# Performance work log

Hardware: AMD Instinct MI355X
Metric: run time of the kernel (lower is better)

The kernel has to match this reference:

```python
import jax, jax.numpy as jnp
import numpy as np

B, S, D = 4, 2048, 512
H = 8
DEPTH = D // H  # 64


def setup_inputs() -> dict:
    key = jax.random.key(0)
    ks = jax.random.split(key, 6)
    scale = 1.0 / np.sqrt(D)
    return {
        "x": jax.random.normal(ks[0], (B, S, D), dtype=jnp.float32),
        "y": jax.random.normal(ks[1], (B, S, D), dtype=jnp.float32),
        "W_q": jax.random.normal(ks[2], (D, D), dtype=jnp.float32) * scale,
        "W_k": jax.random.normal(ks[3], (D, D), dtype=jnp.float32) * scale,
        "W_v": jax.random.normal(ks[4], (D, D), dtype=jnp.float32) * scale,
        "W_o": jax.random.normal(ks[5], (D, D), dtype=jnp.float32) * scale,
    }


def _split_heads(t):
    # [B, S, D] -> [B, H, S, DEPTH]
    b, s, _ = t.shape
    return t.reshape(b, s, H, DEPTH).transpose(0, 2, 1, 3)


def reference(x, y, W_q, W_k, W_v, W_o):
    q = _split_heads(x @ W_q) * (DEPTH ** -0.5)   # [B,H,Sq,d]
    k = _split_heads(y @ W_k)                      # [B,H,Sk,d]
    v = _split_heads(y @ W_v)                      # [B,H,Sk,d]
    logits = jnp.einsum("bhqd,bhkd->bhqk", q, k)   # [B,H,Sq,Sk]
    weights = jax.nn.softmax(logits, axis=-1)
    attn = jnp.einsum("bhqk,bhkd->bhqd", weights, v)  # [B,H,Sq,d]
    attn = attn.transpose(0, 2, 1, 3).reshape(x.shape[0], x.shape[1], D)
    return attn @ W_o
```

## Files before the change

### kernel.cpp

```cpp
#include <hip/hip_runtime.h>
#include <hip/hip_bf16.h>
#include <math.h>
#include <stdint.h>

#define NB 4
#define NS 2048
#define ND 512
#define NH 8
#define DEP 64

typedef __attribute__((ext_vector_type(8))) short bf16x8;
typedef __attribute__((ext_vector_type(4))) short bf16x4;
typedef __attribute__((ext_vector_type(4))) float f32x4;

#define QSCALE 0.18033688011112042f

__device__ __forceinline__ short f2b(float f) {
  unsigned u = __float_as_uint(f);
  u += 0x7FFF + ((u >> 16) & 1);
  return (short)(u >> 16);
}
__device__ __forceinline__ unsigned pk2(float a, float b) {
  union { __hip_bfloat162 h; unsigned u; } c;
  c.h = __float22bfloat162_rn(float2{a, b});
  return c.u;
}

__global__ __launch_bounds__(256) void cast_xy(const float* __restrict__ x,
                                               const float* __restrict__ y,
                                               short* __restrict__ xb,
                                               short* __restrict__ yb) {
  const float* src = blockIdx.y ? y : x;
  short* dst = blockIdx.y ? yb : xb;
  size_t i = ((size_t)blockIdx.x * 256 + threadIdx.x) * 4;
  float4 v = *(const float4*)(src + i);
  bf16x4 o;
  o[0] = f2b(v.x); o[1] = f2b(v.y); o[2] = f2b(v.z); o[3] = f2b(v.w);
  *(bf16x4*)(dst + i) = o;
}

__global__ __launch_bounds__(256) void trans_w(
    const float* __restrict__ W0, const float* __restrict__ W1,
    const float* __restrict__ W2, const float* __restrict__ W3,
    short* __restrict__ T0, short* __restrict__ T1, short* __restrict__ T2,
    short* __restrict__ T3) {
  const float* W = blockIdx.z == 0 ? W0 : blockIdx.z == 1 ? W1
                   : blockIdx.z == 2 ? W2 : W3;
  short* T = blockIdx.z == 0 ? T0 : blockIdx.z == 1 ? T1
             : blockIdx.z == 2 ? T2 : T3;
  __shared__ float tile[64][65];
  const int t = threadIdx.x;
  const int k0 = blockIdx.x * 64, n0 = blockIdx.y * 64;
#pragma unroll
  for (int i = 0; i < 4; ++i) {
    int r = (t >> 4) + i * 16;
    int c = (t & 15) * 4;
    float4 v = *(const float4*)&W[(size_t)(k0 + r) * ND + n0 + c];
    tile[r][c] = v.x; tile[r][c + 1] = v.y;
    tile[r][c + 2] = v.z; tile[r][c + 3] = v.w;
  }
  __syncthreads();
#pragma unroll
  for (int i = 0; i < 4; ++i) {
    int n = (t >> 4) + i * 16;
    int kc = (t & 15) * 4;
    bf16x4 o;
#pragma unroll
    for (int j = 0; j < 4; ++j) o[j] = f2b(tile[kc + j][n]);
    *(bf16x4*)&T[(size_t)(n0 + n) * ND + k0 + kc] = o;
  }
}

__device__ __forceinline__ void gemm_core(const short* __restrict__ A,
                                          const short* __restrict__ Bt,
                                          void* __restrict__ Cout, int mode,
                                          float alpha) {
  __shared__ short As[128 * 72];
  __shared__ short Bs[128 * 72];
  const int t = threadIdx.x;
  const int wave = t >> 6, lane = t & 63;
  const int m = lane & 15, quad = lane >> 4;
  const int m0 = blockIdx.y * 128, n0 = blockIdx.x * 128;
  const int mh = (wave >> 1) * 64, nh = (wave & 1) * 64;
  const int srow = t >> 3, sc8 = (t & 7) * 8;
  f32x4 acc[4][4];
#pragma unroll
  for (int i = 0; i < 4; ++i)
#pragma unroll
    for (int j = 0; j < 4; ++j) acc[i][j] = (f32x4){0.f, 0.f, 0.f, 0.f};

  bf16x8 apre[4], bpre[4];
#pragma unroll
  for (int i = 0; i < 4; ++i) {
    apre[i] = *(const bf16x8*)(A + (size_t)(m0 + srow + i * 32) * ND + sc8);
    bpre[i] = *(const bf16x8*)(Bt + (size_t)(n0 + srow + i * 32) * ND + sc8);
  }

  for (int k0 = 0; k0 < ND; k0 += 64) {
    __syncthreads();
#pragma unroll
    for (int i = 0; i < 4; ++i) {
      *(bf16x8*)(As + (srow + i * 32) * 72 + sc8) = apre[i];
      *(bf16x8*)(Bs + (srow + i * 32) * 72 + sc8) = bpre[i];
    }
    __syncthreads();
    if (k0 + 64 < ND) {
#pragma unroll
      for (int i = 0; i < 4; ++i) {
        apre[i] = *(const bf16x8*)(A + (size_t)(m0 + srow + i * 32) * ND + k0 +
                                   64 + sc8);
        bpre[i] = *(const bf16x8*)(Bt + (size_t)(n0 + srow + i * 32) * ND + k0 +
                                   64 + sc8);
      }
    }
    bf16x8 af[4][2], bf[4][2];
#pragma unroll
    for (int mt = 0; mt < 4; ++mt)
#pragma unroll
      for (int kc = 0; kc < 2; ++kc)
        af[mt][kc] =
            *(const bf16x8*)(As + (mh + mt * 16 + m) * 72 + kc * 32 + quad * 8);
#pragma unroll
    for (int nt = 0; nt < 4; ++nt)
#pragma unroll
      for (int kc = 0; kc < 2; ++kc)
        bf[nt][kc] =
            *(const bf16x8*)(Bs + (nh + nt * 16 + m) * 72 + kc * 32 + quad * 8);
#pragma unroll
    for (int mt = 0; mt < 4; ++mt)
#pragma unroll
      for (int nt = 0; nt < 4; ++nt)
#pragma unroll
        for (int kc = 0; kc < 2; ++kc)
          acc[mt][nt] = __builtin_amdgcn_mfma_f32_16x16x32_bf16(
              af[mt][kc], bf[nt][kc], acc[mt][nt], 0, 0, 0);
  }
  if (mode == 2) {
#pragma unroll
    for (int mt = 0; mt < 4; ++mt)
#pragma unroll
      for (int nt = 0; nt < 4; ++nt) {
        int row0 = m0 + mh + mt * 16 + quad * 4;
        int col = n0 + nh + nt * 16 + m;
        int b_ = row0 >> 11, s_ = row0 & (NS - 1);
        int h_ = col >> 6, d_ = col & (DEP - 1);
        uint2 p;
        p.x = pk2(acc[mt][nt][0] * alpha, acc[mt][nt][1] * alpha);
        p.y = pk2(acc[mt][nt][2] * alpha, acc[mt][nt][3] * alpha);
        *(uint2*)((short*)Cout +
                  (size_t)((b_ * NH + h_) * DEP + d_) * NS + s_) = p;
      }
  } else {
#pragma unroll
    for (int mt = 0; mt < 4; ++mt)
#pragma unroll
      for (int nt = 0; nt < 4; ++nt)
#pragma unroll
        for (int r = 0; r < 4; ++r) {
          int row = m0 + mh + mt * 16 + quad * 4 + r;
          int col = n0 + nh + nt * 16 + m;
          float v = acc[mt][nt][r] * alpha;
          if (mode == 1)
            ((short*)Cout)[(size_t)row * ND + col] = f2b(v);
          else
            ((float*)Cout)[(size_t)row * ND + col] = v;
        }
  }
}

__global__ __launch_bounds__(256) void qkv_gemm(
    const short* __restrict__ xb, const short* __restrict__ yb,
    const short* __restrict__ Wqt, const short* __restrict__ Wkt,
    const short* __restrict__ Wvt, short* __restrict__ Qb,
    short* __restrict__ Kb, short* __restrict__ Vtb) {
  if (blockIdx.z == 0)
    gemm_core(xb, Wqt, Qb, 1, QSCALE);
  else if (blockIdx.z == 1)
    gemm_core(yb, Wkt, Kb, 1, 1.0f);
  else
    gemm_core(yb, Wvt, Vtb, 2, 1.0f);
}

__global__ __launch_bounds__(256) void out_gemm(const short* __restrict__ Ab,
                                                const short* __restrict__ Wot,
                                                float* __restrict__ out) {
  gemm_core(Ab, Wot, out, 0, 1.0f);
}

__global__ __launch_bounds__(256) void attn_mfma(const short* __restrict__ Qb,
                                                 const short* __restrict__ Kb,
                                                 const short* __restrict__ Vtb,
                                                 short* __restrict__ Ob) {
  __shared__ short Ks[64 * 72];
  __shared__ short Vts[64 * 72];
  __shared__ short Pt[128 * 72];
  const int t = threadIdx.x;
  const int wave = t >> 6, lane = t & 63;
  const int m = lane & 15, quad = lane >> 4;
  const int bh = blockIdx.y, b = bh >> 3, h = bh & 7;
  const int q0 = blockIdx.x * 128;
  const int wq = wave * 32;
  const size_t rowb = (size_t)b * NS;
  const short* Vtbase = Vtb + (size_t)(bh * DEP) * NS;
  const int srow = t >> 3, sc8 = (t & 7) * 8;

  bf16x8 qf[2][2];
#pragma unroll
  for (int nt = 0; nt < 2; ++nt)
#pragma unroll
    for (int kc = 0; kc < 2; ++kc)
      qf[nt][kc] = *(const bf16x8*)(Qb + (rowb + q0 + wq + nt * 16 + m) * ND +
                                    h * DEP + kc * 32 + quad * 8);

  float l_[2] = {0.0f, 0.0f};
  f32x4 Ot[4][2];
#pragma unroll
  for (int mt = 0; mt < 4; ++mt)
#pragma unroll
    for (int nt = 0; nt < 2; ++nt) Ot[mt][nt] = (f32x4){0.f, 0.f, 0.f, 0.f};

  bf16x8 kpre[2], vpre[2];
#pragma unroll
  for (int i = 0; i < 2; ++i) {
    kpre[i] =
        *(const bf16x8*)(Kb + (rowb + srow + i * 32) * ND + h * DEP + sc8);
    vpre[i] = *(const bf16x8*)(Vtbase + (size_t)(srow + i * 32) * NS + sc8);
  }

  for (int kv0 = 0; kv0 < NS; kv0 += 64) {
    __syncthreads();
#pragma unroll
    for (int i = 0; i < 2; ++i) {
      *(bf16x8*)(Ks + (srow + i * 32) * 72 + sc8) = kpre[i];
      *(bf16x8*)(Vts + (srow + i * 32) * 72 + sc8) = vpre[i];
    }
    __syncthreads();
    if (kv0 + 64 < NS) {
#pragma unroll
      for (int i = 0; i < 2; ++i) {
        kpre[i] = *(const bf16x8*)(Kb + (rowb + kv0 + 64 + srow + i * 32) * ND +
                                   h * DEP + sc8);
        vpre[i] = *(const bf16x8*)(Vtbase + (size_t)(srow + i * 32) * NS + kv0 +
                                   64 + sc8);
      }
    }

    f32x4 St[4][2];
#pragma unroll
    for (int mt = 0; mt < 4; ++mt)
#pragma unroll
      for (int nt = 0; nt < 2; ++nt) St[mt][nt] = (f32x4){0.f, 0.f, 0.f, 0.f};
#pragma unroll
    for (int mt = 0; mt < 4; ++mt)
#pragma unroll
      for (int kc = 0; kc < 2; ++kc) {
        bf16x8 kf =
            *(const bf16x8*)(Ks + (mt * 16 + m) * 72 + kc * 32 + quad * 8);
#pragma unroll
        for (int nt = 0; nt < 2; ++nt)
          St[mt][nt] = __builtin_amdgcn_mfma_f32_16x16x32_bf16(
              kf, qf[nt][kc], St[mt][nt], 0, 0, 0);
      }

#pragma unroll
    for (int nt = 0; nt < 2; ++nt) {
      float rs = 0.0f;
#pragma unroll
      for (int mt = 0; mt < 4; ++mt) {
        float p0 = exp2f(St[mt][nt][0]);
        float p1 = exp2f(St[mt][nt][1]);
        float p2 = exp2f(St[mt][nt][2]);
        float p3 = exp2f(St[mt][nt][3]);
        rs += (p0 + p1) + (p2 + p3);
        uint2 pk;
        pk.x = pk2(p0, p1);
        pk.y = pk2(p2, p3);
        *(uint2*)(Pt + (wq + nt * 16 + m) * 72 + mt * 16 + quad * 4) = pk;
      }
      l_[nt] += rs;
    }

#pragma unroll
    for (int kc = 0; kc < 2; ++kc) {
      bf16x8 pf[2];
#pragma unroll
      for (int nt = 0; nt < 2; ++nt)
        pf[nt] =
            *(const bf16x8*)(Pt + (wq + nt * 16 + m) * 72 + kc * 32 + quad * 8);
#pragma unroll
      for (int mt = 0; mt < 4; ++mt) {
        bf16x8 vf =
            *(const bf16x8*)(Vts + (mt * 16 + m) * 72 + kc * 32 + quad * 8);
#pragma unroll
        for (int nt = 0; nt < 2; ++nt)
          Ot[mt][nt] = __builtin_amdgcn_mfma_f32_16x16x32_bf16(
              vf, pf[nt], Ot[mt][nt], 0, 0, 0);
      }
    }
  }

#pragma unroll
  for (int nt = 0; nt < 2; ++nt) {
    l_[nt] += __shfl_xor(l_[nt], 16, 64);
    l_[nt] += __shfl_xor(l_[nt], 32, 64);
    float linv = 1.0f / l_[nt];
    size_t row = rowb + q0 + wq + nt * 16 + m;
#pragma unroll
    for (int mt = 0; mt < 4; ++mt)
#pragma unroll
      for (int r = 0; r < 4; ++r)
        Ob[row * ND + h * DEP + mt * 16 + quad * 4 + r] =
            f2b(Ot[mt][nt][r] * linv);
  }
}

extern "C" void kernel_launch(void* const* d_in, const int* in_sizes, int n_in,
                              void* d_out, int out_size, void* d_ws,
                              size_t ws_size, hipStream_t stream) {
  const float* x = (const float*)d_in[0];
  const float* y = (const float*)d_in[1];
  const float* Wq = (const float*)d_in[2];
  const float* Wk = (const float*)d_in[3];
  const float* Wv = (const float*)d_in[4];
  const float* Wo = (const float*)d_in[5];
  float* out = (float*)d_out;

  const size_t mat = (size_t)NB * NS * ND;
  const size_t wsz = (size_t)ND * ND;
  short* xb = (short*)d_ws;
  short* yb = xb + mat;
  short* Wqt = yb + mat;
  short* Wkt = Wqt + wsz;
  short* Wvt = Wkt + wsz;
  short* Wot = Wvt + wsz;
  short* Qb = Wot + wsz;
  short* Kb = Qb + mat;
  short* Vtb = Kb + mat;
  short* attnb = xb;

  cast_xy<<<dim3(mat / 1024, 2), 256, 0, stream>>>(x, y, xb, yb);
  trans_w<<<dim3(8, 8, 4), 256, 0, stream>>>(Wq, Wk, Wv, Wo, Wqt, Wkt, Wvt,
                                             Wot);
  qkv_gemm<<<dim3(ND / 128, (NB * NS) / 128, 3), 256, 0, stream>>>(
      xb, yb, Wqt, Wkt, Wvt, Qb, Kb, Vtb);
  attn_mfma<<<dim3(NS / 128, NB * NH), 256, 0, stream>>>(Qb, Kb, Vtb, attnb);
  out_gemm<<<dim3(ND / 128, (NB * NS) / 128), 256, 0, stream>>>(attnb, Wot,
                                                                out);
}
```

Baseline: 200.7 us.

## Load GEMM and attention tiles via direct global-to-LDS DMA with XOR swizzle

Replaces the register-staged prefetch of A/B (GEMM) and K/Vt (attention) tiles with global_load_lds 16-byte direct-to-LDS transfers. The LDS layout changes from padded stride 72 to unpadded stride 64 with an XOR swizzle, which keeps bank conflicts low. This saves VGPRs and the ds_write instructions. The software prefetch is gone, so each tile load now sits between two barriers and is no longer overlapped with the previous tile's MFMA work. Global latency may become more exposed as a result.

```diff
diff --git a/kernel.cpp b/kernel.cpp
--- a/kernel.cpp
+++ b/kernel.cpp
@@ -24,6 +24,11 @@
   union { __hip_bfloat162 h; unsigned u; } c;
   c.h = __float22bfloat162_rn(float2{a, b});
   return c.u;
+}
+__device__ __forceinline__ void dma16(const void* g, void* l) {
+  __builtin_amdgcn_global_load_lds(
+      (const __attribute__((address_space(1))) void*)g,
+      (__attribute__((address_space(3))) void*)l, 16, 0, 0);
 }
 
 __global__ __launch_bounds__(256) void cast_xy(const float* __restrict__ x,
@@ -75,57 +80,46 @@
                                           const short* __restrict__ Bt,
                                           void* __restrict__ Cout, int mode,
                                           float alpha) {
-  __shared__ short As[128 * 72];
-  __shared__ short Bs[128 * 72];
+  __shared__ short As[128 * 64];
+  __shared__ short Bs[128 * 64];
   const int t = threadIdx.x;
   const int wave = t >> 6, lane = t & 63;
   const int m = lane & 15, quad = lane >> 4;
   const int m0 = blockIdx.y * 128, n0 = blockIdx.x * 128;
   const int mh = (wave >> 1) * 64, nh = (wave & 1) * 64;
-  const int srow = t >> 3, sc8 = (t & 7) * 8;
+  const int r8 = lane >> 3;
+  const int c8 = (lane & 7) ^ r8;
+  const int mx7 = m & 7;
   f32x4 acc[4][4];
 #pragma unroll
   for (int i = 0; i < 4; ++i)
 #pragma unroll
     for (int j = 0; j < 4; ++j) acc[i][j] = (f32x4){0.f, 0.f, 0.f, 0.f};
-
-  bf16x8 apre[4], bpre[4];
-#pragma unroll
-  for (int i = 0; i < 4; ++i) {
-    apre[i] = *(const bf16x8*)(A + (size_t)(m0 + srow + i * 32) * ND + sc8);
-    bpre[i] = *(const bf16x8*)(Bt + (size_t)(n0 + srow + i * 32) * ND + sc8);
-  }
 
   for (int k0 = 0; k0 < ND; k0 += 64) {
     __syncthreads();
 #pragma unroll
     for (int i = 0; i < 4; ++i) {
-      *(bf16x8*)(As + (srow + i * 32) * 72 + sc8) = apre[i];
-      *(bf16x8*)(Bs + (srow + i * 32) * 72 + sc8) = bpre[i];
+      int row = i * 32 + wave * 8 + r8;
+      dma16(A + (size_t)(m0 + row) * ND + k0 + c8 * 8,
+            As + (i * 256 + wave * 64) * 8);
+      dma16(Bt + (size_t)(n0 + row) * ND + k0 + c8 * 8,
+            Bs + (i * 256 + wave * 64) * 8);
     }
     __syncthreads();
-    if (k0 + 64 < ND) {
-#pragma unroll
-      for (int i = 0; i < 4; ++i) {
-        apre[i] = *(const bf16x8*)(A + (size_t)(m0 + srow + i * 32) * ND + k0 +
-                                   64 + sc8);
-        bpre[i] = *(const bf16x8*)(Bt + (size_t)(n0 + srow + i * 32) * ND + k0 +
-                                   64 + sc8);
-      }
-    }
     bf16x8 af[4][2], bf[4][2];
 #pragma unroll
     for (int mt = 0; mt < 4; ++mt)
 #pragma unroll
       for (int kc = 0; kc < 2; ++kc)
-        af[mt][kc] =
-            *(const bf16x8*)(As + (mh + mt * 16 + m) * 72 + kc * 32 + quad * 8);
+        af[mt][kc] = *(const bf16x8*)(As + (mh + mt * 16 + m) * 64 +
+                                      ((kc * 4 + quad) ^ mx7) * 8);
 #pragma unroll
     for (int nt = 0; nt < 4; ++nt)
 #pragma unroll
       for (int kc = 0; kc < 2; ++kc)
-        bf[nt][kc] =
-            *(const bf16x8*)(Bs + (nh + nt * 16 + m) * 72 + kc * 32 + quad * 8);
+        bf[nt][kc] = *(const bf16x8*)(Bs + (nh + nt * 16 + m) * 64 +
+                                      ((kc * 4 + quad) ^ mx7) * 8);
 #pragma unroll
     for (int mt = 0; mt < 4; ++mt)
 #pragma unroll
@@ -191,9 +185,9 @@
                                                  const short* __restrict__ Kb,
                                                  const short* __restrict__ Vtb,
                                                  short* __restrict__ Ob) {
-  __shared__ short Ks[64 * 72];
-  __shared__ short Vts[64 * 72];
-  __shared__ short Pt[128 * 72];
+  __shared__ short Ks[64 * 64];
+  __shared__ short Vts[64 * 64];
+  __shared__ short Pt[128 * 64];
   const int t = threadIdx.x;
   const int wave = t >> 6, lane = t & 63;
   const int m = lane & 15, quad = lane >> 4;
@@ -202,7 +196,9 @@
   const int wq = wave * 32;
   const size_t rowb = (size_t)b * NS;
   const short* Vtbase = Vtb + (size_t)(bh * DEP) * NS;
-  const int srow = t >> 3, sc8 = (t & 7) * 8;
+  const int r8 = lane >> 3;
+  const int c8 = (lane & 7) ^ r8;
+  const int mx7 = m & 7;
 
   bf16x8 qf[2][2];
 #pragma unroll
@@ -219,31 +215,17 @@
 #pragma unroll
     for (int nt = 0; nt < 2; ++nt) Ot[mt][nt] = (f32x4){0.f, 0.f, 0.f, 0.f};
 
-  bf16x8 kpre[2], vpre[2];
-#pragma unroll
-  for (int i = 0; i < 2; ++i) {
-    kpre[i] =
-        *(const bf16x8*)(Kb + (rowb + srow + i * 32) * ND + h * DEP + sc8);
-    vpre[i] = *(const bf16x8*)(Vtbase + (size_t)(srow + i * 32) * NS + sc8);
-  }
-
   for (int kv0 = 0; kv0 < NS; kv0 += 64) {
     __syncthreads();
 #pragma unroll
     for (int i = 0; i < 2; ++i) {
-      *(bf16x8*)(Ks + (srow + i * 32) * 72 + sc8) = kpre[i];
-      *(bf16x8*)(Vts + (srow + i * 32) * 72 + sc8) = vpre[i];
+      int row = i * 32 + wave * 8 + r8;
+      dma16(Kb + (rowb + kv0 + row) * ND + h * DEP + c8 * 8,
+            Ks + (i * 256 + wave * 64) * 8);
+      dma16(Vtbase + (size_t)row * NS + kv0 + c8 * 8,
+            Vts + (i * 256 + wave * 64) * 8);
     }
     __syncthreads();
-    if (kv0 + 64 < NS) {
-#pragma unroll
-      for (int i = 0; i < 2; ++i) {
-        kpre[i] = *(const bf16x8*)(Kb + (rowb + kv0 + 64 + srow + i * 32) * ND +
-                                   h * DEP + sc8);
-        vpre[i] = *(const bf16x8*)(Vtbase + (size_t)(srow + i * 32) * NS + kv0 +
-                                   64 + sc8);
-      }
-    }
 
     f32x4 St[4][2];
 #pragma unroll
@@ -254,8 +236,8 @@
     for (int mt = 0; mt < 4; ++mt)
 #pragma unroll
       for (int kc = 0; kc < 2; ++kc) {
-        bf16x8 kf =
-            *(const bf16x8*)(Ks + (mt * 16 + m) * 72 + kc * 32 + quad * 8);
+        bf16x8 kf = *(const bf16x8*)(Ks + (mt * 16 + m) * 64 +
+                                     ((kc * 4 + quad) ^ mx7) * 8);
 #pragma unroll
         for (int nt = 0; nt < 2; ++nt)
           St[mt][nt] = __builtin_amdgcn_mfma_f32_16x16x32_bf16(
@@ -275,7 +257,8 @@
         uint2 pk;
         pk.x = pk2(p0, p1);
         pk.y = pk2(p2, p3);
-        *(uint2*)(Pt + (wq + nt * 16 + m) * 72 + mt * 16 + quad * 4) = pk;
+        *(uint2*)(Pt + (wq + nt * 16 + m) * 64 +
+                  ((mt * 2 + (quad >> 1)) ^ mx7) * 8 + (quad & 1) * 4) = pk;
       }
       l_[nt] += rs;
     }
@@ -285,12 +268,12 @@
       bf16x8 pf[2];
 #pragma unroll
       for (int nt = 0; nt < 2; ++nt)
-        pf[nt] =
-            *(const bf16x8*)(Pt + (wq + nt * 16 + m) * 72 + kc * 32 + quad * 8);
+        pf[nt] = *(const bf16x8*)(Pt + (wq + nt * 16 + m) * 64 +
+                                  ((kc * 4 + quad) ^ mx7) * 8);
 #pragma unroll
       for (int mt = 0; mt < 4; ++mt) {
-        bf16x8 vf =
-            *(const bf16x8*)(Vts + (mt * 16 + m) * 72 + kc * 32 + quad * 8);
+        bf16x8 vf = *(const bf16x8*)(Vts + (mt * 16 + m) * 64 +
+                                     ((kc * 4 + quad) ^ mx7) * 8);
 #pragma unroll
         for (int nt = 0; nt < 2; ++nt)
           Ot[mt][nt] = __builtin_amdgcn_mfma_f32_16x16x32_bf16(
```

Result: no change. 202.1 us (+0.7%).
